# Kernel optimization log

Measured on AMD Instinct MI355X. Metric: run time of the kernel, lower is better.

## Reference

```python
import jax, jax.numpy as jnp
import numpy as np

TAU_MIN, TAU_MAX = 5.0, 50.0
BOOST = 3.2
DECO_RATE = 0.01

B, I, F, Q = 4096, 1024, 2048, 4

def setup_inputs() -> dict:
    key = jax.random.key(0)
    ks = jax.random.split(key, 12)
    return {
        "inputs": jax.random.normal(ks[0], (B, I), jnp.float32),
        "hidden_state": jax.random.normal(ks[1], (B, F), jnp.float32),
        "W_in": jax.random.normal(ks[2], (I, F), jnp.float32) / np.sqrt(I),
        "b_in": jnp.zeros((F,), jnp.float32),
        "amp_real": jax.random.normal(ks[3], (F, Q), jnp.float32) * 0.1,
        "amp_imag": jax.random.normal(ks[4], (F, Q), jnp.float32) * 0.1,
        "phase": jax.random.uniform(ks[5], (F, Q), jnp.float32, 0.0, 2 * np.pi),
        "primary": jax.random.normal(ks[6], (F, F), jnp.float32) / np.sqrt(F),
        "ent_mat": jax.random.normal(ks[7], (F, F), jnp.float32) / np.sqrt(F),
        "corr": jax.random.uniform(ks[8], (F,), jnp.float32, 0.0, 0.7),
        "W_tau": jax.random.uniform(ks[9], (F, F), jnp.float32, 0.0, 0.1) / np.sqrt(F),
        "b_tau": jnp.zeros((F,), jnp.float32),
        "W_dec": jax.random.uniform(ks[10], (F, F), jnp.float32, 0.0, 0.5) / np.sqrt(F),
        "b_dec": jnp.zeros((F,), jnp.float32),
        "time_step": 1,
    }

def reference(inputs, hidden_state, W_in, b_in, amp_real, amp_imag, phase,
              primary, ent_mat, corr, W_tau, b_tau, W_dec, b_dec, time_step):
    t = jnp.float32(time_step)
    batch = inputs.shape[0]
    feats = hidden_state.shape[1]

    # input projection: [B,I] @ [I,F]
    x_proj = inputs @ W_in + b_in

    # quantum superposition state (batch-independent, [F,Q] params)
    ph = phase + t * 0.1
    real_c = amp_real * jnp.cos(ph)          # [F,Q]
    imag_c = amp_imag * jnp.sin(ph)          # [F,Q]
    sup_r = real_c.sum(-1)                    # [F]
    sup_i = imag_c.sum(-1)                    # [F]
    prob_amp = real_c ** 2 + imag_c ** 2      # [F,Q]
    q_state = sup_r * jnp.exp(-sup_i ** 2)    # [F]
    q_state_b = jnp.broadcast_to(q_state, (batch, feats))
    prob_amp_b = jnp.broadcast_to(prob_amp, (batch,) + prob_amp.shape)

    # entangled recurrent connections: two F x F matmuls
    ent_rec = hidden_state @ primary + (hidden_state @ ent_mat) * corr

    # quantum time constants
    tau_raw = q_state_b @ W_tau + b_tau
    tau_q = (TAU_MIN + (TAU_MAX - TAU_MIN) * jax.nn.sigmoid(tau_raw)) / BOOST

    # decoherence gate
    deco = jax.nn.sigmoid(q_state_b @ W_dec + b_dec)
    coherent = jnp.exp(-DECO_RATE * t)

    classical = jnp.tanh(x_proj + ent_rec)
    quantum_act = q_state_b * deco * coherent
    combined = classical + quantum_act

    dx_dt = (-hidden_state + combined) / tau_q
    dt_q = 0.1 / BOOST
    new_hidden = hidden_state + dt_q * dx_dt

    # diagnostics
    d_amp = jnp.mean(prob_amp_b, axis=-1)          # [B,F]
    d_coh = coherent
    d_ent = jnp.mean(jnp.abs(ent_rec))
    d_dec = jnp.mean(deco)
    d_tau = jnp.mean(tau_q)
    return (new_hidden, d_amp, d_coh, d_ent, d_dec, d_tau)
```

## Files before the change

kernel.cpp:

```cpp
#include <hip/hip_runtime.h>
#include <hip/hip_bf16.h>

#define BD 4096
#define ID 1024
#define FD 2048
#define NT 96

typedef __bf16 v8bf __attribute__((ext_vector_type(8)));
typedef float  v4f  __attribute__((ext_vector_type(4)));

struct alignas(8) bf4 { __hip_bfloat16 x, y, z, w; };

__device__ inline __hip_bfloat16 bf(float f) { return __float2bfloat16(f); }
__device__ inline float sig(float x) { return 1.f / (1.f + expf(-x)); }

__device__ inline void gload16(const __hip_bfloat16* g, __hip_bfloat16* l) {
  __builtin_amdgcn_global_load_lds(
      (const __attribute__((address_space(1))) void*)g,
      (__attribute__((address_space(3))) void*)l, 16, 0, 0);
}

__global__ void k_prep_q(const float* ar, const float* ai, const float* ph,
                         const int* tstep, float* qs, float* pamp,
                         float* scal, float* tau_raw, float* dec_raw) {
  int j = blockIdx.x * 256 + threadIdx.x;
  if (j < 4) scal[j] = 0.f;
  if (j < FD) { tau_raw[j] = 0.f; dec_raw[j] = 0.f; }
  if (j >= FD) return;
  float t = (float)tstep[0];
  float4 a = ((const float4*)ar)[j];
  float4 b = ((const float4*)ai)[j];
  float4 p = ((const float4*)ph)[j];
  float sr = 0.f, si = 0.f, pm = 0.f;
  {
    float c, s, rc, ic;
    c = cosf(p.x + 0.1f * t); s = sinf(p.x + 0.1f * t);
    rc = a.x * c; ic = b.x * s; sr += rc; si += ic; pm += rc * rc + ic * ic;
    c = cosf(p.y + 0.1f * t); s = sinf(p.y + 0.1f * t);
    rc = a.y * c; ic = b.y * s; sr += rc; si += ic; pm += rc * rc + ic * ic;
    c = cosf(p.z + 0.1f * t); s = sinf(p.z + 0.1f * t);
    rc = a.z * c; ic = b.z * s; sr += rc; si += ic; pm += rc * rc + ic * ic;
    c = cosf(p.w + 0.1f * t); s = sinf(p.w + 0.1f * t);
    rc = a.w * c; ic = b.w * s; sr += rc; si += ic; pm += rc * rc + ic * ic;
  }
  qs[j] = sr * expf(-si * si);
  pamp[j] = 0.25f * pm;
}

__global__ void k_cast(const float* s1, __hip_bfloat16* d1, int n1,
                       const float* s2, __hip_bfloat16* d2) {
  int i = blockIdx.x * blockDim.x + threadIdx.x;
  const float* src = s1; __hip_bfloat16* dst = d1;
  if (i >= n1) { i -= n1; src = s2; dst = d2; }
  float4 v = ((const float4*)src)[i];
  bf4 o{bf(v.x), bf(v.y), bf(v.z), bf(v.w)};
  ((bf4*)dst)[i] = o;
}

__global__ void k_tcast(const float* src, const float* src2, const float* corr,
                        __hip_bfloat16* dst, int R, int C, int useM) {
  __shared__ float t[32][33];
  int tx = threadIdx.x, ty = threadIdx.y;
  int x = blockIdx.x * 32 + tx;
  int yb = blockIdx.y * 32;
  float cr = useM ? corr[x] : 0.f;
#pragma unroll
  for (int j = 0; j < 4; j++) {
    int y = yb + ty + j * 8;
    float v = src[(size_t)y * C + x];
    if (useM) v += src2[(size_t)y * C + x] * cr;
    t[ty + j * 8][tx] = v;
  }
  __syncthreads();
#pragma unroll
  for (int j = 0; j < 4; j++) {
    int orow = blockIdx.x * 32 + ty + j * 8;
    int ocol = yb + tx;
    dst[(size_t)orow * R + ocol] = bf(t[tx][ty + j * 8]);
  }
}

__global__ void k_matvec(const float* qs, const float* Wt, const float* Wd,
                         float* tau_raw, float* dec_raw) {
  int j = blockIdx.x * 256 + threadIdx.x;
  int i0 = blockIdx.y * 128;
  const float* W = blockIdx.z ? Wd : Wt;
  float* out = blockIdx.z ? dec_raw : tau_raw;
  __shared__ float q[128];
  if (threadIdx.x < 128) q[threadIdx.x] = qs[i0 + threadIdx.x];
  __syncthreads();
  float acc = 0.f;
#pragma unroll 8
  for (int i = 0; i < 128; i++) acc = fmaf(q[i], W[(size_t)(i0 + i) * FD + j], acc);
  atomicAdd(&out[j], acc);
}

__global__ void k_post(const float* tau_raw, const float* dec_raw, const float* qs,
                       const float* b_tau, const float* b_dec, const int* tstep,
                       float* s_arr, float* qact, float* scal) {
  int j = blockIdx.x * 256 + threadIdx.x;
  float t = (float)tstep[0];
  float coh = expf(-0.01f * t);
  float tq = (5.f + 45.f * sig(tau_raw[j] + b_tau[j])) / 3.2f;
  s_arr[j] = 0.03125f / tq;
  float dec = sig(dec_raw[j] + b_dec[j]);
  qact[j] = qs[j] * dec * coh;
  float tsum = tq, dsum = dec;
  for (int off = 32; off; off >>= 1) {
    tsum += __shfl_down(tsum, off);
    dsum += __shfl_down(dsum, off);
  }
  __shared__ float rt[4], rd[4];
  int w = threadIdx.x >> 6;
  if ((threadIdx.x & 63) == 0) { rt[w] = tsum; rd[w] = dsum; }
  __syncthreads();
  if (threadIdx.x == 0) {
    atomicAdd(&scal[1], rd[0] + rd[1] + rd[2] + rd[3]);
    atomicAdd(&scal[2], rt[0] + rt[1] + rt[2] + rt[3]);
  }
}

__global__ __launch_bounds__(256, 2) void k_gemm(
    const __hip_bfloat16* __restrict__ Ah,
    const __hip_bfloat16* __restrict__ MT,
    const __hip_bfloat16* __restrict__ Ax,
    const __hip_bfloat16* __restrict__ WT,
    const float* __restrict__ b_in, const float* __restrict__ s_arr,
    const float* __restrict__ qact,
    float* ent_sum, float* __restrict__ out) {
  __shared__ alignas(16) __hip_bfloat16 As[3][128][32];
  __shared__ alignas(16) __hip_bfloat16 Bs[3][128][32];
  __shared__ float red[4];

  const int tid = threadIdx.x;
  const int l = tid & 63, w = tid >> 6;
  const int wr = w >> 1, wc = w & 1;
  const int row0 = blockIdx.x * 128, col0 = blockIdx.y * 128;

  v4f acc[4][4];
#pragma unroll
  for (int i = 0; i < 4; i++)
#pragma unroll
    for (int j = 0; j < 4; j++) acc[i][j] = (v4f)0.f;

  const int srow = l >> 2;
  const int scol = ((l & 3) ^ ((l >> 3) & 3)) * 8;
  const int rcol = ((l >> 4) ^ ((l >> 1) & 3)) * 8;

  auto stage = [&](int t) {
    int buf = t % 3;
    const __hip_bfloat16* A = (t < 64) ? Ah : Ax;
    const __hip_bfloat16* B = (t < 64) ? MT : WT;
    int ld = (t < 64) ? FD : ID;
    int k = (t & 63) * 32;
#pragma unroll
    for (int i = 0; i < 2; i++) {
      int rr = w * 32 + i * 16;
      gload16(A + (size_t)(row0 + rr + srow) * ld + k + scol, &As[buf][rr][0]);
      gload16(B + (size_t)(col0 + rr + srow) * ld + k + scol, &Bs[buf][rr][0]);
    }
  };
  auto compute = [&](int t) {
    int buf = t % 3;
    v8bf a[4], b[4];
#pragma unroll
    for (int mi = 0; mi < 4; mi++)
      a[mi] = *(const v8bf*)&As[buf][wr * 64 + mi * 16 + (l & 15)][rcol];
#pragma unroll
    for (int ni = 0; ni < 4; ni++)
      b[ni] = *(const v8bf*)&Bs[buf][wc * 64 + ni * 16 + (l & 15)][rcol];
#pragma unroll
    for (int mi = 0; mi < 4; mi++)
#pragma unroll
      for (int ni = 0; ni < 4; ni++)
        acc[mi][ni] = __builtin_amdgcn_mfma_f32_16x16x32_bf16(a[mi], b[ni], acc[mi][ni], 0, 0, 0);
  };

  stage(0);
  __builtin_amdgcn_sched_barrier(0);
  stage(1);

  float asum = 0.f;

  for (int t = 0; t < NT - 1; t++) {
    asm volatile("s_waitcnt vmcnt(4)" ::: "memory");
    __builtin_amdgcn_s_barrier();
    __builtin_amdgcn_sched_barrier(0);
    if (t + 2 < NT) stage(t + 2);
    compute(t);
    if (t == 63) {
#pragma unroll
      for (int mi = 0; mi < 4; mi++)
#pragma unroll
        for (int ni = 0; ni < 4; ni++)
#pragma unroll
          for (int e = 0; e < 4; e++) asum += fabsf(acc[mi][ni][e]);
    }
  }
  asm volatile("s_waitcnt vmcnt(0)" ::: "memory");
  __builtin_amdgcn_s_barrier();
  __builtin_amdgcn_sched_barrier(0);
  compute(NT - 1);

  for (int off = 32; off; off >>= 1) asum += __shfl_down(asum, off);
  if (l == 0) red[w] = asum;
  __syncthreads();
  if (tid == 0) atomicAdd(ent_sum, red[0] + red[1] + red[2] + red[3]);

#pragma unroll
  for (int ni = 0; ni < 4; ni++) {
    int gc = col0 + wc * 64 + ni * 16 + (l & 15);
    float bi = b_in[gc], qa = qact[gc], sj = s_arr[gc];
#pragma unroll
    for (int mi = 0; mi < 4; mi++) {
      int gr0 = row0 + wr * 64 + mi * 16 + (l >> 4) * 4;
#pragma unroll
      for (int e = 0; e < 4; e++) {
        int gr = gr0 + e;
        float comb = tanhf(acc[mi][ni][e] + bi) + qa;
        float h = __bfloat162float(Ah[(size_t)gr * FD + gc]);
        out[(size_t)gr * FD + gc] = fmaf(sj, comb - h, h);
      }
    }
  }
}

__global__ void k_damp(const float* __restrict__ pamp, const float* scal,
                       const int* tstep, float* __restrict__ out1, float* out3) {
  int i = blockIdx.x * 256 + threadIdx.x;
  int c = (i * 4) & (FD - 1);
  ((float4*)out1)[i] = *(const float4*)&pamp[c];
  if (i == 0) {
    float t = (float)tstep[0];
    out3[0] = expf(-0.01f * t);
    out3[1] = scal[0] / (float)((size_t)BD * FD);
    out3[2] = scal[1] / (float)FD;
    out3[3] = scal[2] / (float)FD;
  }
}

extern "C" void kernel_launch(void* const* d_in, const int* in_sizes, int n_in,
                              void* d_out, int out_size, void* d_ws, size_t ws_size,
                              hipStream_t stream) {
  const float* inputs  = (const float*)d_in[0];
  const float* hidden  = (const float*)d_in[1];
  const float* W_in    = (const float*)d_in[2];
  const float* b_in    = (const float*)d_in[3];
  const float* amp_r   = (const float*)d_in[4];
  const float* amp_i   = (const float*)d_in[5];
  const float* phase   = (const float*)d_in[6];
  const float* primary = (const float*)d_in[7];
  const float* ent_mat = (const float*)d_in[8];
  const float* corr    = (const float*)d_in[9];
  const float* W_tau   = (const float*)d_in[10];
  const float* b_tau   = (const float*)d_in[11];
  const float* W_dec   = (const float*)d_in[12];
  const float* b_dec   = (const float*)d_in[13];
  const int*   tstep   = (const int*)d_in[14];

  char* ws = (char*)d_ws;
  __hip_bfloat16* inputs_bf = (__hip_bfloat16*)(ws + 0);
  __hip_bfloat16* hidden_bf = (__hip_bfloat16*)(ws + 8388608);
  __hip_bfloat16* WT        = (__hip_bfloat16*)(ws + 25165824);
  __hip_bfloat16* MT        = (__hip_bfloat16*)(ws + 29360128);
  char* sb = ws + 37748736;
  float* scal    = (float*)(sb);
  float* qs      = (float*)(sb + 16);
  float* pamp    = (float*)(sb + 16 + 8192);
  float* tau_raw = (float*)(sb + 16 + 2 * 8192);
  float* dec_raw = (float*)(sb + 16 + 3 * 8192);
  float* s_arr   = (float*)(sb + 16 + 4 * 8192);
  float* qact    = (float*)(sb + 16 + 5 * 8192);

  float* out = (float*)d_out;

  hipLaunchKernelGGL(k_prep_q, dim3(8), dim3(256), 0, stream,
                     amp_r, amp_i, phase, tstep, qs, pamp, scal, tau_raw, dec_raw);
  hipLaunchKernelGGL(k_cast, dim3(12288), dim3(256), 0, stream,
                     inputs, inputs_bf, BD * ID / 4, hidden, hidden_bf);
  hipLaunchKernelGGL(k_tcast, dim3(64, 32), dim3(32, 8), 0, stream,
                     W_in, (const float*)nullptr, (const float*)nullptr, WT, ID, FD, 0);
  hipLaunchKernelGGL(k_tcast, dim3(64, 64), dim3(32, 8), 0, stream,
                     primary, ent_mat, corr, MT, FD, FD, 1);
  hipLaunchKernelGGL(k_matvec, dim3(8, 16, 2), dim3(256), 0, stream, qs, W_tau, W_dec, tau_raw, dec_raw);
  hipLaunchKernelGGL(k_post, dim3(8), dim3(256), 0, stream, tau_raw, dec_raw, qs, b_tau, b_dec, tstep, s_arr, qact, scal);
  hipLaunchKernelGGL(k_gemm, dim3(32, 16), dim3(256), 0, stream,
                     hidden_bf, MT, inputs_bf, WT, b_in, s_arr, qact,
                     &scal[0], out);
  hipLaunchKernelGGL(k_damp, dim3(8192), dim3(256), 0, stream,
                     pamp, scal, tstep, out + (size_t)BD * FD, out + (size_t)2 * BD * FD);
}
```

Baseline: 147.1 us.

## Split K of fused GEMM into three partial GEMMs plus combine kernel

Splits the concatenated-K GEMM into three independent grid slices (two halves of the hidden@M K range, and the input projection), each writing bf16 partial results to workspace. A new combine kernel sums the partials, applies tanh, bias and the state update, writes d_amp, and finalizes the scalar diagnostics with a last-block counter. The aim is to triple the block count to fill more CUs and raise occupancy, at the cost of extra global traffic for bf16 intermediates and an extra launch. It falls back to the old fused path when the workspace is too small. The ent reduction now uses bf16-rounded partials, so precision changes slightly.

```diff
diff --git a/kernel.cpp b/kernel.cpp
--- a/kernel.cpp
+++ b/kernel.cpp
@@ -4,7 +4,6 @@
 #define BD 4096
 #define ID 1024
 #define FD 2048
-#define NT 96
 
 typedef __bf16 v8bf __attribute__((ext_vector_type(8)));
 typedef float  v4f  __attribute__((ext_vector_type(4)));
@@ -120,22 +119,27 @@
   }
 }
 
-__global__ __launch_bounds__(256, 2) void k_gemm(
+__global__ __launch_bounds__(256, 4) void k_gemm_split(
     const __hip_bfloat16* __restrict__ Ah,
     const __hip_bfloat16* __restrict__ MT,
     const __hip_bfloat16* __restrict__ Ax,
     const __hip_bfloat16* __restrict__ WT,
-    const float* __restrict__ b_in, const float* __restrict__ s_arr,
-    const float* __restrict__ qact,
-    float* ent_sum, float* __restrict__ out) {
-  __shared__ alignas(16) __hip_bfloat16 As[3][128][32];
-  __shared__ alignas(16) __hip_bfloat16 Bs[3][128][32];
-  __shared__ float red[4];
+    __hip_bfloat16* __restrict__ g0, __hip_bfloat16* __restrict__ g1,
+    __hip_bfloat16* __restrict__ gx) {
+  __shared__ alignas(16) __hip_bfloat16 As[2][128][32];
+  __shared__ alignas(16) __hip_bfloat16 Bs[2][128][32];
 
   const int tid = threadIdx.x;
   const int l = tid & 63, w = tid >> 6;
   const int wr = w >> 1, wc = w & 1;
   const int row0 = blockIdx.x * 128, col0 = blockIdx.y * 128;
+  const int bz = blockIdx.z;
+
+  const __hip_bfloat16* A = (bz < 2) ? Ah : Ax;
+  const __hip_bfloat16* B = (bz < 2) ? MT : WT;
+  const int ld = (bz < 2) ? FD : ID;
+  const int kb = (bz == 1) ? 1024 : 0;
+  __hip_bfloat16* gout = (bz == 0) ? g0 : (bz == 1) ? g1 : gx;
 
   v4f acc[4][4];
 #pragma unroll
@@ -147,6 +151,121 @@
   const int scol = ((l & 3) ^ ((l >> 3) & 3)) * 8;
   const int rcol = ((l >> 4) ^ ((l >> 1) & 3)) * 8;
 
+  auto stage = [&](int buf, int kt) {
+    int k = kb + kt * 32;
+#pragma unroll
+    for (int i = 0; i < 2; i++) {
+      int rr = w * 32 + i * 16;
+      gload16(A + (size_t)(row0 + rr + srow) * ld + k + scol, &As[buf][rr][0]);
+      gload16(B + (size_t)(col0 + rr + srow) * ld + k + scol, &Bs[buf][rr][0]);
+    }
+  };
+  auto compute = [&](int buf) {
+    v8bf a[4], b[4];
+#pragma unroll
+    for (int mi = 0; mi < 4; mi++)
+      a[mi] = *(const v8bf*)&As[buf][wr * 64 + mi * 16 + (l & 15)][rcol];
+#pragma unroll
+    for (int ni = 0; ni < 4; ni++)
+      b[ni] = *(const v8bf*)&Bs[buf][wc * 64 + ni * 16 + (l & 15)][rcol];
+#pragma unroll
+    for (int mi = 0; mi < 4; mi++)
+#pragma unroll
+      for (int ni = 0; ni < 4; ni++)
+        acc[mi][ni] = __builtin_amdgcn_mfma_f32_16x16x32_bf16(a[mi], b[ni], acc[mi][ni], 0, 0, 0);
+  };
+
+  stage(0, 0);
+  __syncthreads();
+  for (int kt = 0; kt < 32; kt++) {
+    if (kt + 1 < 32) stage((kt + 1) & 1, kt + 1);
+    compute(kt & 1);
+    __syncthreads();
+  }
+
+#pragma unroll
+  for (int ni = 0; ni < 4; ni++) {
+    int gc = col0 + wc * 64 + ni * 16 + (l & 15);
+#pragma unroll
+    for (int mi = 0; mi < 4; mi++) {
+      int gr0 = row0 + wr * 64 + mi * 16 + (l >> 4) * 4;
+#pragma unroll
+      for (int e = 0; e < 4; e++)
+        gout[(size_t)(gr0 + e) * FD + gc] = bf(acc[mi][ni][e]);
+    }
+  }
+}
+
+__global__ __launch_bounds__(256) void k_comb(
+    const __hip_bfloat16* __restrict__ g0, const __hip_bfloat16* __restrict__ g1,
+    const __hip_bfloat16* __restrict__ gx, const float* __restrict__ hidden,
+    const float* __restrict__ b_in, const float* __restrict__ s_arr,
+    const float* __restrict__ qact, const float* __restrict__ pamp,
+    const int* tstep, float* scal, float* __restrict__ out) {
+  const int row = blockIdx.x;
+  const int c = threadIdx.x * 8;
+  const size_t base = (size_t)row * FD + c;
+  v8bf a0 = *(const v8bf*)(g0 + base);
+  v8bf a1 = *(const v8bf*)(g1 + base);
+  v8bf axv = *(const v8bf*)(gx + base);
+  float4 h0 = *(const float4*)(hidden + base);
+  float4 h1 = *(const float4*)(hidden + base + 4);
+  float asum = 0.f;
+  float o[8];
+#pragma unroll
+  for (int j = 0; j < 8; j++) {
+    float e = (float)a0[j] + (float)a1[j];
+    asum += fabsf(e);
+    float g = e + (float)axv[j] + b_in[c + j];
+    float comb = tanhf(g) + qact[c + j];
+    float h = (j < 4) ? (&h0.x)[j] : (&h1.x)[j - 4];
+    o[j] = fmaf(s_arr[c + j], comb - h, h);
+  }
+  *(float4*)&out[base] = make_float4(o[0], o[1], o[2], o[3]);
+  *(float4*)&out[base + 4] = make_float4(o[4], o[5], o[6], o[7]);
+  *(float4*)&out[(size_t)BD * FD + base] = *(const float4*)&pamp[c];
+  *(float4*)&out[(size_t)BD * FD + base + 4] = *(const float4*)&pamp[c + 4];
+
+  for (int off = 32; off; off >>= 1) asum += __shfl_down(asum, off);
+  __shared__ float red[4];
+  if ((threadIdx.x & 63) == 0) red[threadIdx.x >> 6] = asum;
+  __syncthreads();
+  if (threadIdx.x == 0) {
+    atomicAdd(&scal[0], red[0] + red[1] + red[2] + red[3]);
+    __threadfence();
+    int* cnt = (int*)(scal + 3);
+    if (atomicAdd(cnt, 1) == (int)gridDim.x - 1) {
+      float tot = atomicAdd(&scal[0], 0.f);
+      float t = (float)tstep[0];
+      float* o3 = out + (size_t)2 * BD * FD;
+      o3[0] = expf(-0.01f * t);
+      o3[1] = tot / (float)((size_t)BD * FD);
+      o3[2] = scal[1] / (float)FD;
+      o3[3] = scal[2] / (float)FD;
+    }
+  }
+}
+
+__global__ __launch_bounds__(256, 2) void k_gemm_fused(
+    const __hip_bfloat16* __restrict__ Ah, const __hip_bfloat16* __restrict__ MT,
+    const __hip_bfloat16* __restrict__ Ax, const __hip_bfloat16* __restrict__ WT,
+    const float* __restrict__ b_in, const float* __restrict__ s_arr,
+    const float* __restrict__ qact, float* ent_sum, float* __restrict__ out) {
+  __shared__ alignas(16) __hip_bfloat16 As[3][128][32];
+  __shared__ alignas(16) __hip_bfloat16 Bs[3][128][32];
+  __shared__ float red[4];
+  const int tid = threadIdx.x;
+  const int l = tid & 63, w = tid >> 6;
+  const int wr = w >> 1, wc = w & 1;
+  const int row0 = blockIdx.x * 128, col0 = blockIdx.y * 128;
+  v4f acc[4][4];
+#pragma unroll
+  for (int i = 0; i < 4; i++)
+#pragma unroll
+    for (int j = 0; j < 4; j++) acc[i][j] = (v4f)0.f;
+  const int srow = l >> 2;
+  const int scol = ((l & 3) ^ ((l >> 3) & 3)) * 8;
+  const int rcol = ((l >> 4) ^ ((l >> 1) & 3)) * 8;
   auto stage = [&](int t) {
     int buf = t % 3;
     const __hip_bfloat16* A = (t < 64) ? Ah : Ax;
@@ -175,18 +294,15 @@
       for (int ni = 0; ni < 4; ni++)
         acc[mi][ni] = __builtin_amdgcn_mfma_f32_16x16x32_bf16(a[mi], b[ni], acc[mi][ni], 0, 0, 0);
   };
-
   stage(0);
   __builtin_amdgcn_sched_barrier(0);
   stage(1);
-
   float asum = 0.f;
-
-  for (int t = 0; t < NT - 1; t++) {
+  for (int t = 0; t < 95; t++) {
     asm volatile("s_waitcnt vmcnt(4)" ::: "memory");
     __builtin_amdgcn_s_barrier();
     __builtin_amdgcn_sched_barrier(0);
-    if (t + 2 < NT) stage(t + 2);
+    if (t + 2 < 96) stage(t + 2);
     compute(t);
     if (t == 63) {
 #pragma unroll
@@ -200,13 +316,11 @@
   asm volatile("s_waitcnt vmcnt(0)" ::: "memory");
   __builtin_amdgcn_s_barrier();
   __builtin_amdgcn_sched_barrier(0);
-  compute(NT - 1);
-
+  compute(95);
   for (int off = 32; off; off >>= 1) asum += __shfl_down(asum, off);
   if (l == 0) red[w] = asum;
   __syncthreads();
   if (tid == 0) atomicAdd(ent_sum, red[0] + red[1] + red[2] + red[3]);
-
 #pragma unroll
   for (int ni = 0; ni < 4; ni++) {
     int gc = col0 + wc * 64 + ni * 16 + (l & 15);
@@ -263,7 +377,12 @@
   __hip_bfloat16* hidden_bf = (__hip_bfloat16*)(ws + 8388608);
   __hip_bfloat16* WT        = (__hip_bfloat16*)(ws + 25165824);
   __hip_bfloat16* MT        = (__hip_bfloat16*)(ws + 29360128);
-  char* sb = ws + 37748736;
+  __hip_bfloat16* g0        = (__hip_bfloat16*)(ws + 37748736);
+  __hip_bfloat16* g1        = (__hip_bfloat16*)(ws + 54525952);
+  __hip_bfloat16* gx        = (__hip_bfloat16*)(ws + 71303168);
+
+  const int use_split = (ws_size >= (size_t)88080384 + 65536);
+  char* sb = ws + (use_split ? 88080384 : 37748736);
   float* scal    = (float*)(sb);
   float* qs      = (float*)(sb + 16);
   float* pamp    = (float*)(sb + 16 + 8192);
@@ -284,9 +403,18 @@
                      primary, ent_mat, corr, MT, FD, FD, 1);
   hipLaunchKernelGGL(k_matvec, dim3(8, 16, 2), dim3(256), 0, stream, qs, W_tau, W_dec, tau_raw, dec_raw);
   hipLaunchKernelGGL(k_post, dim3(8), dim3(256), 0, stream, tau_raw, dec_raw, qs, b_tau, b_dec, tstep, s_arr, qact, scal);
-  hipLaunchKernelGGL(k_gemm, dim3(32, 16), dim3(256), 0, stream,
-                     hidden_bf, MT, inputs_bf, WT, b_in, s_arr, qact,
-                     &scal[0], out);
-  hipLaunchKernelGGL(k_damp, dim3(8192), dim3(256), 0, stream,
-                     pamp, scal, tstep, out + (size_t)BD * FD, out + (size_t)2 * BD * FD);
-}
+
+  if (use_split) {
+    hipLaunchKernelGGL(k_gemm_split, dim3(32, 16, 3), dim3(256), 0, stream,
+                       hidden_bf, MT, inputs_bf, WT, g0, g1, gx);
+    hipLaunchKernelGGL(k_comb, dim3(4096), dim3(256), 0, stream,
+                       g0, g1, gx, hidden, b_in, s_arr, qact, pamp, tstep,
+                       scal, out);
+  } else {
+    hipLaunchKernelGGL(k_gemm_fused, dim3(32, 16), dim3(256), 0, stream,
+                       hidden_bf, MT, inputs_bf, WT, b_in, s_arr, qact,
+                       &scal[0], out);
+    hipLaunchKernelGGL(k_damp, dim3(8192), dim3(256), 0, stream,
+                       pamp, scal, tstep, out + (size_t)BD * FD, out + (size_t)2 * BD * FD);
+  }
+}
```

New measurement: 329.6 us. +124.1%, slower.
